# Kernel optimization log

Measured on AMD Instinct MI355X. Metric: run time of the kernel, lower is better.

The kernel has to match this reference:

```python
import jax, jax.numpy as jnp
import numpy as np

B, T, C, H, D = 4, 2048, 1024, 16, 64  # batch, seq, n_embd, n_head, head_size


def setup_inputs() -> dict:
    key = jax.random.key(0)
    ks = jax.random.split(key, 8)
    s = 0.02  # init scale for weights
    return {
        "q": jax.random.normal(ks[0], (B, T, C), jnp.float32),
        "k": jax.random.normal(ks[1], (B, T, C), jnp.float32),
        "v": jax.random.normal(ks[2], (B, T, C), jnp.float32),
        "Wq": jax.random.normal(ks[3], (H, C, D), jnp.float32) * s,
        "Wk": jax.random.normal(ks[4], (H, C, D), jnp.float32) * s,
        "Wv": jax.random.normal(ks[5], (H, C, D), jnp.float32) * s,
        "Wo": jax.random.normal(ks[6], (H * D, C), jnp.float32) * s,
        "bo": jnp.zeros((C,), jnp.float32),
    }


def reference(q, k, v, Wq, Wk, Wv, Wo, bo):
    # Per-head projections (vectorized over heads): [B,T,C] x [H,C,D] -> [B,H,T,D]
    qh = jnp.einsum('btc,hcd->bhtd', q, Wq)
    kh = jnp.einsum('btc,hcd->bhtd', k, Wk)
    vh = jnp.einsum('btc,hcd->bhtd', v, Wv)
    # NOTE: source divides by sqrt(C) = sqrt(n_embd), not sqrt(head_size)
    scale = 1.0 / jnp.sqrt(jnp.float32(C))
    att = jnp.einsum('bhtd,bhsd->bhts', qh, kh) * scale  # [B,H,T,T]
    causal = jnp.tril(jnp.ones((T, T), dtype=bool))
    att = jnp.where(causal, att, -jnp.inf)
    p = jax.nn.softmax(att, axis=-1)  # dropout is identity in eval mode
    out = jnp.einsum('bhts,bhsd->bhtd', p, vh)
    # concat heads in order: [B,H,T,D] -> [B,T,H*D]
    out = out.transpose(0, 2, 1, 3).reshape(B, T, H * D)
    return out @ Wo + bo
```

## Files before the change

kernel.cpp:

```cpp
#include <hip/hip_runtime.h>
#include <hip/hip_bf16.h>
#include <cstdint>
#include <cstddef>

#define B_  4
#define T_  2048
#define C_  1024
#define H_  16
#define D_  64
#define MROWS (B_*T_)
#define NDIM  (H_*D_)

typedef float  f32x4 __attribute__((ext_vector_type(4)));
typedef __bf16 bfrag __attribute__((ext_vector_type(8)));

__device__ __forceinline__ unsigned short f2bf(float f) {
  union { float f; unsigned u; } v; v.f = f;
  unsigned r = v.u + 0x7fffu + ((v.u >> 16) & 1u);
  return (unsigned short)(r >> 16);
}

__device__ __forceinline__ void async_load16(const void* g, void* l) {
  __builtin_amdgcn_global_load_lds((__attribute__((address_space(1))) void*)(void*)g,
                                   (__attribute__((address_space(3))) void*)l,
                                   16, 0, 0);
}

__device__ __forceinline__ unsigned cvt_pk_bf16(float f0, float f1) {
  unsigned r;
  asm("v_cvt_pk_bf16_f32 %0, %1, %2" : "=v"(r) : "v"(f0), "v"(f1));
  return r;
}

__global__ __launch_bounds__(256) void prep_kernel(
    const float* __restrict__ q, const float* __restrict__ k, const float* __restrict__ v,
    unsigned short* __restrict__ qb, unsigned short* __restrict__ kb, unsigned short* __restrict__ vb,
    const float* __restrict__ Wq, const float* __restrict__ Wk, const float* __restrict__ Wv,
    unsigned short* __restrict__ wqT, unsigned short* __restrict__ wkT, unsigned short* __restrict__ wvT,
    const float* __restrict__ Wo, unsigned short* __restrict__ woT)
{
  const int id = blockIdx.x, tid = threadIdx.x;
  if (id < 24576) {
    int z = id >> 13, blk = id & 8191;
    const float* in = z == 0 ? q : z == 1 ? k : v;
    unsigned short* out = z == 0 ? qb : z == 1 ? kb : vb;
    int i = (blk * 256 + tid) * 4;
    float4 vv = *(const float4*)(in + i);
    ushort4 r;
    r.x = f2bf(vv.x); r.y = f2bf(vv.y); r.z = f2bf(vv.z); r.w = f2bf(vv.w);
    *(ushort4*)(out + i) = r;
  } else if (id < 25344) {
    int u = id - 24576;
    int z = u >> 4, cblk = u & 15;
    int sel = z >> 4, h = z & 15;
    const float* in = (sel == 0 ? Wq : sel == 1 ? Wk : Wv) + (size_t)h * C_ * D_;
    unsigned short* out = (sel == 0 ? wqT : sel == 1 ? wkT : wvT) + (size_t)h * D_ * C_;
    __shared__ float tile[64][65];
    int c0 = cblk * 64;
    int x = tid & 63, y4 = tid >> 6;
    for (int r = y4; r < 64; r += 4)
      tile[r][x] = in[(size_t)(c0 + r) * D_ + x];
    __syncthreads();
    for (int r = y4; r < 64; r += 4)
      out[(size_t)r * C_ + c0 + x] = f2bf(tile[x][r]);
  } else {
    int u = id - 25344;
    __shared__ float tile[64][65];
    int i0 = (u >> 4) * 64, j0 = (u & 15) * 64;
    int x = tid & 63, y4 = tid >> 6;
    for (int r = y4; r < 64; r += 4)
      tile[r][x] = Wo[(size_t)(i0 + r) * C_ + j0 + x];
    __syncthreads();
    for (int r = y4; r < 64; r += 4)
      woT[(size_t)(j0 + r) * NDIM + i0 + x] = f2bf(tile[x][r]);
  }
}

template <int EPI>
__global__ __launch_bounds__(512, 4) void gemm_bt2(
    const unsigned short* __restrict__ A0, const unsigned short* __restrict__ A1, const unsigned short* __restrict__ A2,
    const unsigned short* __restrict__ B0, const unsigned short* __restrict__ B1, const unsigned short* __restrict__ B2,
    void* C0, void* C1, void* C2, const float* __restrict__ bias)
{
  constexpr int K = C_;
  constexpr int N = NDIM;
  __shared__ __align__(16) short As[256 * 64];
  __shared__ __align__(16) short Bs[128 * 64];

  const int id = blockIdx.x;
  const int xcd = id & 7, s = id >> 3;
  const int z = s >> 5;
  const int t = s & 31;
  const int mb = xcd * 4 + (t >> 3);
  const int nb = t & 7;

  const unsigned short* A  = z == 0 ? A0 : z == 1 ? A1 : A2;
  const unsigned short* Bt = z == 0 ? B0 : z == 1 ? B1 : B2;
  void* Cv                 = z == 0 ? C0 : z == 1 ? C1 : C2;

  const int tid = threadIdx.x, lane = tid & 63, wave = tid >> 6;
  const int quad = lane >> 4, l15 = lane & 15;
  const int m0 = mb * 256, n0 = nb * 128;
  const int wm = (wave >> 1) * 64, wn = (wave & 1) * 64;
  const int wbase = tid & ~63;

  f32x4 acc[4][4] = {};

  for (int k0 = 0; k0 < K; k0 += 64) {
#pragma unroll
    for (int i = 0; i < 4; ++i) {
      int p0 = i * 512 + wbase;
      int p = p0 + lane;
      int m = p >> 3, cl = (p & 7) ^ (m & 7);
      async_load16(A + (size_t)(m0 + m) * K + k0 + cl * 8, (char*)As + p0 * 16);
    }
#pragma unroll
    for (int i = 0; i < 2; ++i) {
      int p0 = i * 512 + wbase;
      int p = p0 + lane;
      int m = p >> 3, cl = (p & 7) ^ (m & 7);
      async_load16(Bt + (size_t)(n0 + m) * K + k0 + cl * 8, (char*)Bs + p0 * 16);
    }
    __syncthreads();
#pragma unroll
    for (int ks = 0; ks < 2; ++ks) {
      bfrag af[4], bf[4];
#pragma unroll
      for (int i = 0; i < 4; ++i) {
        int m = wm + i * 16 + l15;
        int c = (ks * 4 + quad) ^ (m & 7);
        af[i] = *(const bfrag*)(As + m * 64 + c * 8);
        int n = wn + i * 16 + l15;
        int c2 = (ks * 4 + quad) ^ (n & 7);
        bf[i] = *(const bfrag*)(Bs + n * 64 + c2 * 8);
      }
#pragma unroll
      for (int i = 0; i < 4; ++i)
#pragma unroll
        for (int j = 0; j < 4; ++j)
          acc[i][j] = __builtin_amdgcn_mfma_f32_16x16x32_bf16(af[i], bf[j], acc[i][j], 0, 0, 0);
    }
    __syncthreads();
  }

  if constexpr (EPI == 0) {
    if (z < 2) {
      const float sc = (z == 0) ? 0.045084220f : 1.0f;
      unsigned short* Cb = (unsigned short*)Cv;
#pragma unroll
      for (int i = 0; i < 4; ++i) {
        int row0 = m0 + wm + i * 16 + quad * 4;
#pragma unroll
        for (int j = 0; j < 4; ++j) {
          int col = n0 + wn + j * 16 + l15;
#pragma unroll
          for (int r = 0; r < 4; ++r)
            Cb[(size_t)(row0 + r) * N + col] = f2bf(acc[i][j][r] * sc);
        }
      }
    } else {
      unsigned short* Vo = (unsigned short*)Cv;
#pragma unroll
      for (int i = 0; i < 4; ++i) {
        int m = m0 + wm + i * 16 + quad * 4;
        int bb = m >> 11, tt = m & 2047;
#pragma unroll
        for (int j = 0; j < 4; ++j) {
          int n = n0 + wn + j * 16 + l15;
          int hh = n >> 6, dd = n & 63;
          ushort4 pk;
          pk.x = f2bf(acc[i][j][0]); pk.y = f2bf(acc[i][j][1]);
          pk.z = f2bf(acc[i][j][2]); pk.w = f2bf(acc[i][j][3]);
          *(ushort4*)(Vo + (((size_t)bb * 16 + hh) * 64 + dd) * T_ + tt) = pk;
        }
      }
    }
  } else {
    float* Cf = (float*)Cv;
#pragma unroll
    for (int j = 0; j < 4; ++j) {
      int col = n0 + wn + j * 16 + l15;
      float bv = bias[col];
#pragma unroll
      for (int i = 0; i < 4; ++i) {
        int row0 = m0 + wm + i * 16 + quad * 4;
#pragma unroll
        for (int r = 0; r < 4; ++r)
          Cf[(size_t)(row0 + r) * N + col] = acc[i][j][r] + bv;
      }
    }
  }
}

__global__ __launch_bounds__(256, 3) void flash_kernel(
    const unsigned short* __restrict__ Qh, const unsigned short* __restrict__ Kh,
    const unsigned short* __restrict__ VT, unsigned short* __restrict__ Oh)
{
  __shared__ __align__(16) short Ks[128 * 64];
  __shared__ __align__(16) short Vt[2][64 * 64];
  __shared__ __align__(16) short Ps[4][32 * 72];

  const int tid = threadIdx.x, lane = tid & 63, wave = tid >> 6;
  const int quad = lane >> 4, l15 = lane & 15;
  const int id = blockIdx.x;
  const int rr = id >> 8, cc = id & 255, g = cc >> 6, bh = cc & 63;
  const int t = (rr == 0) ? g : (rr == 1) ? 7 - g : (rr == 2) ? 8 + g : 15 - g;
  const int b = bh >> 4, h = bh & 15;
  const int q0 = t * 128;

  const unsigned short* Qbase = Qh + (size_t)b * T_ * NDIM + h * 64;
  const unsigned short* Kbase = Kh + (size_t)b * T_ * NDIM + h * 64;
  const unsigned short* Vbase = VT + ((size_t)(b * 16 + h) * 64) * T_;

  const int wrow_lo = q0 + wave * 32;

  bfrag qfr[2][2];
#pragma unroll
  for (int j = 0; j < 2; ++j)
#pragma unroll
    for (int ks = 0; ks < 2; ++ks)
      qfr[j][ks] = *(const bfrag*)(Qbase + (size_t)(wrow_lo + j * 16 + l15) * NDIM + ks * 32 + quad * 8);

  float l_st[2] = {0.f, 0.f};
  f32x4 o_acc[2][4] = {};
  short* pw = &Ps[wave][0];

  for (int kv0 = 0; kv0 < q0 + 128; kv0 += 128) {
#pragma unroll
    for (int i = 0; i < 4; ++i) {
      int p0 = (wave * 4 + i) * 64;
      int p = p0 + lane;
      int kr = p >> 3, kcl = (p & 7) ^ (kr & 7);
      async_load16(Kbase + (size_t)(kv0 + kr) * NDIM + kcl * 8, (char*)Ks + p0 * 16);
      int hh = p >> 9, d = (p >> 3) & 63, vcl = (p & 7) ^ (d & 7);
      async_load16(Vbase + (size_t)d * T_ + kv0 + hh * 64 + vcl * 8, (char*)Vt + p0 * 16);
    }
    __syncthreads();

#pragma unroll
    for (int hf = 0; hf < 2; ++hf) {
      const int kvh = kv0 + hf * 64;
      if (kvh > wrow_lo + 31) break;

      f32x4 sv[2][4] = {};
#pragma unroll
      for (int ks = 0; ks < 2; ++ks) {
        bfrag kf[4];
#pragma unroll
        for (int i = 0; i < 4; ++i) {
          int key = i * 16 + l15;
          int c = (ks * 4 + quad) ^ (key & 7);
          kf[i] = *(const bfrag*)(Ks + (hf * 64 + key) * 64 + c * 8);
        }
#pragma unroll
        for (int j = 0; j < 2; ++j)
#pragma unroll
          for (int i = 0; i < 4; ++i)
            sv[j][i] = __builtin_amdgcn_mfma_f32_16x16x32_bf16(kf[i], qfr[j][ks], sv[j][i], 0, 0, 0);
      }

#pragma unroll
      for (int j = 0; j < 2; ++j)
#pragma unroll
        for (int i = 0; i < 4; ++i)
#pragma unroll
          for (int r = 0; r < 4; ++r)
            sv[j][i][r] = __builtin_amdgcn_exp2f(sv[j][i][r]);
      if (kvh + 63 > wrow_lo) {
#pragma unroll
        for (int j = 0; j < 2; ++j) {
          int qr = wrow_lo + j * 16 + l15;
#pragma unroll
          for (int i = 0; i < 4; ++i) {
            int keyb = kvh + i * 16 + quad * 4;
#pragma unroll
            for (int r = 0; r < 4; ++r)
              if (keyb + r > qr) sv[j][i][r] = 0.f;
          }
        }
      }

#pragma unroll
      for (int j = 0; j < 2; ++j) {
#pragma unroll
        for (int i = 0; i < 4; ++i) {
          l_st[j] += sv[j][i][0] + sv[j][i][1] + sv[j][i][2] + sv[j][i][3];
          uint2 pk;
          pk.x = cvt_pk_bf16(sv[j][i][0], sv[j][i][1]);
          pk.y = cvt_pk_bf16(sv[j][i][2], sv[j][i][3]);
          *(uint2*)(pw + (j * 16 + l15) * 72 + i * 16 + quad * 4) = pk;
        }
      }

#pragma unroll
      for (int ks = 0; ks < 2; ++ks) {
        bfrag vf[4], pf[2];
#pragma unroll
        for (int i2 = 0; i2 < 4; ++i2) {
          int d = i2 * 16 + l15;
          int c = (ks * 4 + quad) ^ (d & 7);
          vf[i2] = *(const bfrag*)(&Vt[hf][0] + d * 64 + c * 8);
        }
#pragma unroll
        for (int j = 0; j < 2; ++j)
          pf[j] = *(const bfrag*)(pw + (j * 16 + l15) * 72 + ks * 32 + quad * 8);
#pragma unroll
        for (int j = 0; j < 2; ++j)
#pragma unroll
          for (int i2 = 0; i2 < 4; ++i2)
            o_acc[j][i2] = __builtin_amdgcn_mfma_f32_16x16x32_bf16(vf[i2], pf[j], o_acc[j][i2], 0, 0, 0);
      }
    }
    __syncthreads();
  }

#pragma unroll
  for (int j = 0; j < 2; ++j) {
    float s = l_st[j];
    s += __shfl_xor(s, 16, 64);
    s += __shfl_xor(s, 32, 64);
    float inv = 1.f / s;
    int qr = q0 + wave * 32 + j * 16 + l15;
    size_t base = ((size_t)b * T_ + qr) * NDIM + h * 64;
#pragma unroll
    for (int i2 = 0; i2 < 4; ++i2) {
      uint2 pk;
      pk.x = cvt_pk_bf16(o_acc[j][i2][0] * inv, o_acc[j][i2][1] * inv);
      pk.y = cvt_pk_bf16(o_acc[j][i2][2] * inv, o_acc[j][i2][3] * inv);
      *(uint2*)(Oh + base + i2 * 16 + quad * 4) = pk;
    }
  }
}

extern "C" void kernel_launch(void* const* d_in, const int* in_sizes, int n_in,
                              void* d_out, int out_size, void* d_ws, size_t ws_size,
                              hipStream_t stream)
{
  const float* q  = (const float*)d_in[0];
  const float* k  = (const float*)d_in[1];
  const float* v  = (const float*)d_in[2];
  const float* Wq = (const float*)d_in[3];
  const float* Wk = (const float*)d_in[4];
  const float* Wv = (const float*)d_in[5];
  const float* Wo = (const float*)d_in[6];
  const float* bo = (const float*)d_in[7];
  float* out = (float*)d_out;

  char* w = (char*)d_ws;
  const size_t szBTC = (size_t)MROWS * C_ * 2;
  const size_t szW   = (size_t)NDIM * C_ * 2;
  unsigned short* qb   = (unsigned short*)(w);
  unsigned short* kb   = (unsigned short*)(w + szBTC);
  unsigned short* vb   = (unsigned short*)(w + 2 * szBTC);
  unsigned short* wqT  = (unsigned short*)(w + 3 * szBTC);
  unsigned short* wkT  = (unsigned short*)(w + 3 * szBTC + szW);
  unsigned short* wvT  = (unsigned short*)(w + 3 * szBTC + 2 * szW);
  unsigned short* woT  = (unsigned short*)(w + 3 * szBTC + 3 * szW);
  unsigned short* qhp  = (unsigned short*)(w + 3 * szBTC + 4 * szW);
  unsigned short* khp  = (unsigned short*)(w + 4 * szBTC + 4 * szW);
  unsigned short* vT   = (unsigned short*)(w + 5 * szBTC + 4 * szW);
  unsigned short* attO = (unsigned short*)(w + 6 * szBTC + 4 * szW);

  prep_kernel<<<dim3(25600), 256, 0, stream>>>(q, k, v, qb, kb, vb,
                                               Wq, Wk, Wv, wqT, wkT, wvT, Wo, woT);

  gemm_bt2<0><<<dim3(768), 512, 0, stream>>>(
      qb, kb, vb, wqT, wkT, wvT, qhp, khp, vT, nullptr);

  flash_kernel<<<dim3(1024), 256, 0, stream>>>(qhp, khp, vT, attO);

  gemm_bt2<1><<<dim3(256), 512, 0, stream>>>(
      attO, attO, attO, woT, woT, woT, out, out, out, bo);
}
```

Baseline: 295.6 us.

## Give output projection its own smaller-tile GEMM and batch prep conversion per block

The output projection GEMM, previously launched as 256 blocks of 512 threads with 256x128 tiles, now runs in a dedicated kernel with 128x128 tiles, 256 threads and 512 blocks. The goal is to fill more compute units for this small GEMM. The fp32-to-bf16 input conversion in the prep kernel now handles eight float4 chunks per thread in 3072 blocks instead of 24576, cutting block-launch overhead. Smaller tiles reload operands more often across blocks, and fewer prep blocks lower available parallelism.

```diff
diff --git a/kernel.cpp b/kernel.cpp
--- a/kernel.cpp
+++ b/kernel.cpp
@@ -40,17 +40,21 @@
     const float* __restrict__ Wo, unsigned short* __restrict__ woT)
 {
   const int id = blockIdx.x, tid = threadIdx.x;
-  if (id < 24576) {
-    int z = id >> 13, blk = id & 8191;
+  if (id < 3072) {
+    int z = id >> 10, blk = id & 1023;
     const float* in = z == 0 ? q : z == 1 ? k : v;
     unsigned short* out = z == 0 ? qb : z == 1 ? kb : vb;
-    int i = (blk * 256 + tid) * 4;
-    float4 vv = *(const float4*)(in + i);
-    ushort4 r;
-    r.x = f2bf(vv.x); r.y = f2bf(vv.y); r.z = f2bf(vv.z); r.w = f2bf(vv.w);
-    *(ushort4*)(out + i) = r;
-  } else if (id < 25344) {
-    int u = id - 24576;
+    int base = blk * 2048;
+#pragma unroll
+    for (int r2 = 0; r2 < 8; ++r2) {
+      int i = (base + r2 * 256 + tid) * 4;
+      float4 vv = *(const float4*)(in + i);
+      ushort4 rr;
+      rr.x = f2bf(vv.x); rr.y = f2bf(vv.y); rr.z = f2bf(vv.z); rr.w = f2bf(vv.w);
+      *(ushort4*)(out + i) = rr;
+    }
+  } else if (id < 3840) {
+    int u = id - 3072;
     int z = u >> 4, cblk = u & 15;
     int sel = z >> 4, h = z & 15;
     const float* in = (sel == 0 ? Wq : sel == 1 ? Wk : Wv) + (size_t)h * C_ * D_;
@@ -64,7 +68,7 @@
     for (int r = y4; r < 64; r += 4)
       out[(size_t)r * C_ + c0 + x] = f2bf(tile[x][r]);
   } else {
-    int u = id - 25344;
+    int u = id - 3840;
     __shared__ float tile[64][65];
     int i0 = (u >> 4) * 64, j0 = (u & 15) * 64;
     int x = tid & 63, y4 = tid >> 6;
@@ -76,11 +80,10 @@
   }
 }
 
-template <int EPI>
-__global__ __launch_bounds__(512, 4) void gemm_bt2(
+__global__ __launch_bounds__(512, 4) void gemm_qkv(
     const unsigned short* __restrict__ A0, const unsigned short* __restrict__ A1, const unsigned short* __restrict__ A2,
     const unsigned short* __restrict__ B0, const unsigned short* __restrict__ B1, const unsigned short* __restrict__ B2,
-    void* C0, void* C1, void* C2, const float* __restrict__ bias)
+    void* C0, void* C1, void* C2)
 {
   constexpr int K = C_;
   constexpr int N = NDIM;
@@ -143,51 +146,101 @@
     __syncthreads();
   }
 
-  if constexpr (EPI == 0) {
-    if (z < 2) {
-      const float sc = (z == 0) ? 0.045084220f : 1.0f;
-      unsigned short* Cb = (unsigned short*)Cv;
+  if (z < 2) {
+    const float sc = (z == 0) ? 0.045084220f : 1.0f;
+    unsigned short* Cb = (unsigned short*)Cv;
+#pragma unroll
+    for (int i = 0; i < 4; ++i) {
+      int row0 = m0 + wm + i * 16 + quad * 4;
+#pragma unroll
+      for (int j = 0; j < 4; ++j) {
+        int col = n0 + wn + j * 16 + l15;
+#pragma unroll
+        for (int r = 0; r < 4; ++r)
+          Cb[(size_t)(row0 + r) * N + col] = f2bf(acc[i][j][r] * sc);
+      }
+    }
+  } else {
+    unsigned short* Vo = (unsigned short*)Cv;
+#pragma unroll
+    for (int i = 0; i < 4; ++i) {
+      int m = m0 + wm + i * 16 + quad * 4;
+      int bb = m >> 11, tt = m & 2047;
+#pragma unroll
+      for (int j = 0; j < 4; ++j) {
+        int n = n0 + wn + j * 16 + l15;
+        int hh = n >> 6, dd = n & 63;
+        ushort4 pk;
+        pk.x = f2bf(acc[i][j][0]); pk.y = f2bf(acc[i][j][1]);
+        pk.z = f2bf(acc[i][j][2]); pk.w = f2bf(acc[i][j][3]);
+        *(ushort4*)(Vo + (((size_t)bb * 16 + hh) * 64 + dd) * T_ + tt) = pk;
+      }
+    }
+  }
+}
+
+__global__ __launch_bounds__(256) void gemm_o(
+    const unsigned short* __restrict__ A, const unsigned short* __restrict__ Bt,
+    float* __restrict__ Cf, const float* __restrict__ bias)
+{
+  constexpr int K = NDIM;
+  constexpr int N = C_;
+  __shared__ __align__(16) short As[128 * 64];
+  __shared__ __align__(16) short Bs[128 * 64];
+
+  const int id = blockIdx.x;
+  const int xcd = id & 7, t = id >> 3;
+  const int mb = xcd * 8 + (t >> 3);
+  const int nb = t & 7;
+
+  const int tid = threadIdx.x, lane = tid & 63, wave = tid >> 6;
+  const int quad = lane >> 4, l15 = lane & 15;
+  const int m0 = mb * 128, n0 = nb * 128;
+  const int wm = (wave >> 1) * 64, wn = (wave & 1) * 64;
+
+  f32x4 acc[4][4] = {};
+
+  for (int k0 = 0; k0 < K; k0 += 64) {
+#pragma unroll
+    for (int i = 0; i < 4; ++i) {
+      int p0 = (wave * 4 + i) * 64;
+      int p = p0 + lane;
+      int m = p >> 3, cl = (p & 7) ^ (m & 7);
+      async_load16(A  + (size_t)(m0 + m) * K + k0 + cl * 8, (char*)As + p0 * 16);
+      async_load16(Bt + (size_t)(n0 + m) * K + k0 + cl * 8, (char*)Bs + p0 * 16);
+    }
+    __syncthreads();
+#pragma unroll
+    for (int ks = 0; ks < 2; ++ks) {
+      bfrag af[4], bf[4];
 #pragma unroll
       for (int i = 0; i < 4; ++i) {
-        int row0 = m0 + wm + i * 16 + quad * 4;
-#pragma unroll
-        for (int j = 0; j < 4; ++j) {
-          int col = n0 + wn + j * 16 + l15;
-#pragma unroll
-          for (int r = 0; r < 4; ++r)
-            Cb[(size_t)(row0 + r) * N + col] = f2bf(acc[i][j][r] * sc);
-        }
-      }
-    } else {
-      unsigned short* Vo = (unsigned short*)Cv;
-#pragma unroll
-      for (int i = 0; i < 4; ++i) {
-        int m = m0 + wm + i * 16 + quad * 4;
-        int bb = m >> 11, tt = m & 2047;
-#pragma unroll
-        for (int j = 0; j < 4; ++j) {
-          int n = n0 + wn + j * 16 + l15;
-          int hh = n >> 6, dd = n & 63;
-          ushort4 pk;
-          pk.x = f2bf(acc[i][j][0]); pk.y = f2bf(acc[i][j][1]);
-          pk.z = f2bf(acc[i][j][2]); pk.w = f2bf(acc[i][j][3]);
-          *(ushort4*)(Vo + (((size_t)bb * 16 + hh) * 64 + dd) * T_ + tt) = pk;
-        }
-      }
-    }
-  } else {
-    float* Cf = (float*)Cv;
-#pragma unroll
-    for (int j = 0; j < 4; ++j) {
-      int col = n0 + wn + j * 16 + l15;
-      float bv = bias[col];
-#pragma unroll
-      for (int i = 0; i < 4; ++i) {
-        int row0 = m0 + wm + i * 16 + quad * 4;
-#pragma unroll
-        for (int r = 0; r < 4; ++r)
-          Cf[(size_t)(row0 + r) * N + col] = acc[i][j][r] + bv;
-      }
+        int m = wm + i * 16 + l15;
+        int c = (ks * 4 + quad) ^ (m & 7);
+        af[i] = *(const bfrag*)(As + m * 64 + c * 8);
+        int n = wn + i * 16 + l15;
+        int c2 = (ks * 4 + quad) ^ (n & 7);
+        bf[i] = *(const bfrag*)(Bs + n * 64 + c2 * 8);
+      }
+#pragma unroll
+      for (int i = 0; i < 4; ++i)
+#pragma unroll
+        for (int j = 0; j < 4; ++j)
+          acc[i][j] = __builtin_amdgcn_mfma_f32_16x16x32_bf16(af[i], bf[j], acc[i][j], 0, 0, 0);
+    }
+    __syncthreads();
+  }
+
+#pragma unroll
+  for (int j = 0; j < 4; ++j) {
+    int col = n0 + wn + j * 16 + l15;
+    float bv = bias[col];
+#pragma unroll
+    for (int i = 0; i < 4; ++i) {
+      int row0 = m0 + wm + i * 16 + quad * 4;
+#pragma unroll
+      for (int r = 0; r < 4; ++r)
+        Cf[(size_t)(row0 + r) * N + col] = acc[i][j][r] + bv;
     }
   }
 }
@@ -361,14 +414,13 @@
   unsigned short* vT   = (unsigned short*)(w + 5 * szBTC + 4 * szW);
   unsigned short* attO = (unsigned short*)(w + 6 * szBTC + 4 * szW);
 
-  prep_kernel<<<dim3(25600), 256, 0, stream>>>(q, k, v, qb, kb, vb,
-                                               Wq, Wk, Wv, wqT, wkT, wvT, Wo, woT);
-
-  gemm_bt2<0><<<dim3(768), 512, 0, stream>>>(
-      qb, kb, vb, wqT, wkT, wvT, qhp, khp, vT, nullptr);
+  prep_kernel<<<dim3(4096), 256, 0, stream>>>(q, k, v, qb, kb, vb,
+                                              Wq, Wk, Wv, wqT, wkT, wvT, Wo, woT);
+
+  gemm_qkv<<<dim3(768), 512, 0, stream>>>(
+      qb, kb, vb, wqT, wkT, wvT, qhp, khp, vT);
 
   flash_kernel<<<dim3(1024), 256, 0, stream>>>(qhp, khp, vT, attO);
 
-  gemm_bt2<1><<<dim3(256), 512, 0, stream>>>(
-      attO, attO, attO, woT, woT, woT, out, out, out, bo);
-}
+  gemm_o<<<dim3(512), 256, 0, stream>>>(attO, woT, out, bo);
+}
```

New measurement: 307.7 us. 4.1% more time.
